# Kernel optimization log

Measured on AMD Instinct MI355X. Metric: run time of the kernel, lower is better.

## Reference

```python
import jax, jax.numpy as jnp
import numpy as np

NH = 16  # num_attention_heads
DH = 64  # attention_head_size
HID = NH * DH
TYPE_VOCAB = 2


def setup_inputs() -> dict:
    key = jax.random.key(0)
    ks = jax.random.split(key, 10)
    B, S = 4, 2048
    s = 0.02
    return {
        "hidden_states": jax.random.normal(ks[0], (B, S, HID), jnp.float32),
        "attention_mask": jnp.zeros((B, 1, 1, S), jnp.float32),
        "seg_ids": jax.random.randint(ks[1], (B, S), 0, TYPE_VOCAB),
        "Wq": jax.random.normal(ks[2], (HID, HID), jnp.float32) * s,
        "bq": jnp.zeros((HID,), jnp.float32),
        "Wk": jax.random.normal(ks[3], (HID, HID), jnp.float32) * s,  # key has NO bias (F.linear with weight only)
        "Wv": jax.random.normal(ks[4], (HID, HID), jnp.float32) * s,
        "bv": jnp.zeros((HID,), jnp.float32),
        "seg_table": jax.random.normal(ks[5], (TYPE_VOCAB, HID), jnp.float32) * s,
        "b_q_s": jnp.zeros((1, NH, 1, DH), jnp.float32),
    }


def reference(hidden_states, attention_mask, seg_ids, Wq, bq, Wk, Wv, bv, seg_table, b_q_s):
    B, S, H = hidden_states.shape
    # QKV projections (key projection has no bias, matching F.linear(x, key.weight))
    q = hidden_states @ Wq.T + bq
    k = hidden_states @ Wk.T
    v = hidden_states @ Wv.T + bv
    # [B, NH, S, DH]
    q = q.reshape(B, S, NH, DH).transpose(0, 2, 1, 3)
    k = k.reshape(B, S, NH, DH).transpose(0, 2, 1, 3)
    v = v.reshape(B, S, NH, DH).transpose(0, 2, 1, 3)
    scale = 1.0 / np.sqrt(DH).astype(np.float32)
    scores = jnp.einsum('bhid,bhjd->bhij', q * scale, k)
    # segment-embedding bias: seg_rep [B, S, NH, DH]
    seg_rep = seg_table[seg_ids].reshape(B, S, NH, DH)
    qs = jnp.einsum('bhid,bjhd->bhij', q + b_q_s, seg_rep)
    scores = scores + qs + attention_mask
    probs = jax.nn.softmax(scores, axis=-1)  # dropout: eval mode (identity)
    ctx = jnp.einsum('bhij,bhjd->bihd', probs, v).reshape(B, S, H)
    return ctx
```

## Files before the change

### kernel.cpp

```cpp
#include <hip/hip_runtime.h>
#include <cstdint>
#include <cmath>

#define RLN2 1.44269504088896340736f

typedef __attribute__((ext_vector_type(8))) short short8;
typedef __attribute__((ext_vector_type(4))) float f32x4;
typedef __attribute__((ext_vector_type(4))) unsigned int uint4v;

__device__ __forceinline__ unsigned short f2bf(float f) {
  unsigned int u = __float_as_uint(f);
  u += 0x7fffu + ((u >> 16) & 1u);
  return (unsigned short)(u >> 16);
}

__device__ __forceinline__ unsigned int cvt_pk_bf16(float lo, float hi) {
  unsigned int r;
  asm("v_cvt_pk_bf16_f32 %0, %1, %2" : "=v"(r) : "v"(lo), "v"(hi));
  return r;
}

__device__ __forceinline__ float fast_exp2(float x) {
#if __has_builtin(__builtin_amdgcn_exp2f)
  return __builtin_amdgcn_exp2f(x);
#else
  return exp2f(x);
#endif
}

__device__ __forceinline__ void gload16(const void* g, void* l) {
  __builtin_amdgcn_global_load_lds(
      (const __attribute__((address_space(1))) unsigned int*)g,
      (__attribute__((address_space(3))) unsigned int*)l,
      16, 0, 0);
}


__global__ void __launch_bounds__(256) k_cvt_hs(const float* __restrict__ src,
                                                unsigned short* __restrict__ dst) {
  size_t i = (size_t)blockIdx.x * 256 + threadIdx.x;
  const float4* s = (const float4*)src + i * 2;
  float4 a = s[0], b = s[1];
  short8 o;
  o[0] = (short)f2bf(a.x); o[1] = (short)f2bf(a.y); o[2] = (short)f2bf(a.z); o[3] = (short)f2bf(a.w);
  o[4] = (short)f2bf(b.x); o[5] = (short)f2bf(b.y); o[6] = (short)f2bf(b.z); o[7] = (short)f2bf(b.w);
  ((short8*)dst)[i] = o;
}

__global__ void __launch_bounds__(256) k_cvt_w(const float* __restrict__ Wq,
                                               const float* __restrict__ Wk,
                                               const float* __restrict__ Wv,
                                               unsigned short* __restrict__ dst) {
  size_t i = (size_t)blockIdx.x * 256 + threadIdx.x;
  int e = (int)(i * 8);
  int n = e >> 10, c = e & 1023;
  const float* row = (n < 1024) ? (Wq + (size_t)n * 1024)
                   : (n < 2048) ? (Wk + (size_t)(n - 1024) * 1024)
                                : (Wv + (size_t)(n - 2048) * 1024);
  const float4* s = (const float4*)(row + c);
  float4 a = s[0], b = s[1];
  short8 o;
  o[0] = (short)f2bf(a.x); o[1] = (short)f2bf(a.y); o[2] = (short)f2bf(a.z); o[3] = (short)f2bf(a.w);
  o[4] = (short)f2bf(b.x); o[5] = (short)f2bf(b.y); o[6] = (short)f2bf(b.z); o[7] = (short)f2bf(b.w);
  ((short8*)dst)[i] = o;
}

__global__ void __launch_bounds__(256) k_seg(const int* __restrict__ seg_ids,
                                             const float* __restrict__ seg_table,
                                             unsigned short* __restrict__ Kaug) {
  size_t i = (size_t)blockIdx.x * 256 + threadIdx.x;
  int e = (int)(i * 8);
  int jl = e >> 10;
  int r  = e & 1023;
  int sid = seg_ids[jl];
  const float4* s = (const float4*)(seg_table + (size_t)sid * 1024 + r);
  float4 a = s[0], b = s[1];
  short8 o;
  o[0] = (short)f2bf(a.x); o[1] = (short)f2bf(a.y); o[2] = (short)f2bf(a.z); o[3] = (short)f2bf(a.w);
  o[4] = (short)f2bf(b.x); o[5] = (short)f2bf(b.y); o[6] = (short)f2bf(b.z); o[7] = (short)f2bf(b.w);
  int b_ = jl >> 11, j = jl & 2047;
  int h = r >> 6, d = r & 63;
  size_t off = ((size_t)(b_ * 16 + h) * 2048 + j) * 128 + 64 + d;
  *(short8*)(Kaug + off) = o;
}

__global__ void __launch_bounds__(256) k_vt(const unsigned short* __restrict__ V,
                                            unsigned short* __restrict__ Vt) {
  __shared__ unsigned short lt[64 * 72];
  int blk = blockIdx.x;
  int bh = blk >> 5, jt = blk & 31;
  int j0 = jt * 64;
  int tid = threadIdx.x;
  const char* src = (const char*)(V + ((size_t)bh * 2048 + j0) * 64);
#pragma unroll
  for (int it = 0; it < 2; ++it) {
    int c = tid + it * 256;
    int j = c >> 3, colb = (c & 7) * 16;
    int jpos = (j & 32) | ((((j >> 2) & 3) << 3) + (((j >> 4) & 1) << 2) + (j & 3));
    short8 v = *(const short8*)(src + (size_t)j * 128 + colb);
    int d0 = colb >> 1;
#pragma unroll
    for (int e = 0; e < 8; ++e)
      lt[(d0 + e) * 72 + jpos] = (unsigned short)v[e];
  }
  __syncthreads();
  char* dst = (char*)(Vt + (size_t)bh * 131072 + j0);
#pragma unroll
  for (int it = 0; it < 2; ++it) {
    int c = tid + it * 256;
    int d = c >> 3, jc = (c & 7) * 8;
    short8 o = *(const short8*)&lt[d * 72 + jc];
    *(short8*)(dst + (size_t)d * 4096 + jc * 2) = o;
  }
}

__global__ void __launch_bounds__(256) k_gemm(const unsigned short* __restrict__ A,
                                              const unsigned short* __restrict__ Bw,
                                              const float* __restrict__ bq,
                                              const float* __restrict__ bv,
                                              const float* __restrict__ bqs,
                                              unsigned short* __restrict__ Qaug,
                                              unsigned short* __restrict__ Kaug,
                                              unsigned short* __restrict__ Vo) {
  __shared__ unsigned short As[128 * 32];
  __shared__ unsigned short Bs[128 * 32];
  int n0 = blockIdx.x * 128;
  int m0 = blockIdx.y * 128;
  int tid = threadIdx.x;
  int w = tid >> 6, lane = tid & 63;
  int wr = (w >> 1) * 64, wc = (w & 1) * 64;
  int rA = lane & 15;
  int kg = (lane >> 4) * 16;
  f32x4 acc[4][4] = {};
  const char* Ab = (const char*)A;
  const char* Bb = (const char*)Bw;

  for (int kt = 0; kt < 32; ++kt) {
    int kb0 = kt * 64;
#pragma unroll
    for (int c = 0; c < 2; ++c) {
      int chunk = w * 2 + c;
      int y = chunk * 1024 + lane * 16;
      int row = y >> 6, colb = y & 63;
      gload16(Ab + (size_t)(m0 + row) * 2048 + kb0 + colb, (char*)As + chunk * 1024);
      gload16(Bb + (size_t)(n0 + row) * 2048 + kb0 + colb, (char*)Bs + chunk * 1024);
    }
    __syncthreads();
    short8 af[4], bfr[4];
#pragma unroll
    for (int m = 0; m < 4; ++m)
      af[m] = *(const short8*)((const char*)As + (wr + m * 16 + rA) * 64 + kg);
#pragma unroll
    for (int n = 0; n < 4; ++n)
      bfr[n] = *(const short8*)((const char*)Bs + (wc + n * 16 + rA) * 64 + kg);
#pragma unroll
    for (int m = 0; m < 4; ++m)
#pragma unroll
      for (int n = 0; n < 4; ++n)
        acc[m][n] = __builtin_amdgcn_mfma_f32_16x16x32_bf16(af[m], bfr[n], acc[m][n], 0, 0, 0);
    __syncthreads();
  }

  int seg = n0 >> 10;
  int colbase = n0 & 1023;
#pragma unroll
  for (int n = 0; n < 4; ++n) {
    int o = colbase + wc + n * 16 + (lane & 15);
    int h = o >> 6, d = o & 63;
    float bias = 0.f, bqsv = 0.f;
    if (seg == 0) { bias = bq[o]; bqsv = bqs[o]; }
    else if (seg == 2) { bias = bv[o]; }
#pragma unroll
    for (int m = 0; m < 4; ++m) {
#pragma unroll
      for (int r = 0; r < 4; ++r) {
        int i = m0 + wr + m * 16 + (lane >> 4) * 4 + r;
        int b_ = i >> 11, sdx = i & 2047;
        float val = acc[m][n][r];
        size_t tok = (size_t)(b_ * 16 + h) * 2048 + sdx;
        if (seg == 0) {
          float qv = val + bias;
          Qaug[tok * 128 + d]      = f2bf(qv * (0.125f * RLN2));
          Qaug[tok * 128 + 64 + d] = f2bf((qv + bqsv) * RLN2);
        } else if (seg == 1) {
          Kaug[tok * 128 + d] = f2bf(val);
        } else {
          Vo[tok * 64 + d] = f2bf(val + bias);
        }
      }
    }
  }
}

__global__ void __launch_bounds__(256, 3) k_attn(const unsigned short* __restrict__ Qaug,
                                                 const unsigned short* __restrict__ Kaug,
                                                 const unsigned short* __restrict__ Vt,
                                                 const float* __restrict__ mask,
                                                 float* __restrict__ out) {
  __shared__ char smem[49152];
  char* Ksb = smem;
  char* Vsb = smem + 32768;

  int qt = blockIdx.x, h = blockIdx.y, b_ = blockIdx.z;
  int bh = b_ * 16 + h;
  int i0 = qt * 64;
  int tid = threadIdx.x, w = tid >> 6, lane = tid & 63;
  int q16 = lane & 15, g = lane >> 4;
  int swzq = (q16 & 7) << 4;
  const char* Qg = (const char*)Qaug + (size_t)bh * 2048 * 256;
  const char* Kg = (const char*)Kaug + (size_t)bh * 2048 * 256;
  const char* Vg = (const char*)Vt + (size_t)bh * 64 * 4096;
  const float* maskb = mask + (size_t)b_ * 2048;

  int kl_row = lane >> 2, kl_cb = (lane & 3) * 16;
  int vl_dvl = lane >> 3, vl_bv = (lane & 7) * 16;

#pragma unroll
  for (int c = 0; c < 4; ++c) {
    int ck = w * 4 + c;
    int db = ck >> 2, rhi = (ck & 3) << 4;
    gload16(Kg + (size_t)(rhi + kl_row) * 256 + db * 64 + kl_cb, Ksb + ck * 1024);
  }
#pragma unroll
  for (int c = 0; c < 2; ++c) {
    int ck = w * 2 + c;
    int dv = ck * 8 + vl_dvl;
    gload16(Vg + (size_t)dv * 4096 + ((vl_bv ^ ((dv & 7) << 4)) & 127), Vsb + ck * 1024);
  }

  short8 qf[4];
  {
    const char* qrow = Qg + (size_t)(i0 + w * 16 + q16) * 256 + g * 16;
#pragma unroll
    for (int db = 0; db < 4; ++db)
      qf[db] = *(const short8*)(qrow + db * 64);
  }
  __syncthreads();

  float m_run = -1e30f, l_run = 0.f;
  f32x4 accO[4] = {};

  for (int t = 0; t < 32; ++t) {
    int cur = t & 1, nxt = cur ^ 1;
    int j0 = t * 64;
    if (t < 31) {
      int jn = j0 + 64;
      char* kd = Ksb + nxt * 16384;
      char* vd = Vsb + nxt * 8192;
#pragma unroll
      for (int c = 0; c < 4; ++c) {
        int ck = w * 4 + c;
        int db = ck >> 2, rhi = (ck & 3) << 4;
        gload16(Kg + (size_t)(jn + rhi + kl_row) * 256 + db * 64 + kl_cb, kd + ck * 1024);
      }
#pragma unroll
      for (int c = 0; c < 2; ++c) {
        int ck = w * 2 + c;
        int dv = ck * 8 + vl_dvl;
        gload16(Vg + (size_t)dv * 4096 + jn * 2 + ((vl_bv ^ ((dv & 7) << 4)) & 127),
                vd + ck * 1024);
      }
    }
    const char* kbase = Ksb + cur * 16384 + q16 * 64 + g * 16;
    const char* vb_ = Vsb + cur * 8192;
    const char* vbase0 = vb_ + ((q16 * 128 + g * 16) ^ swzq);
    const char* vbase1 = vb_ + ((q16 * 128 + 64 + g * 16) ^ swzq);

    f32x4 s[4] = {};
    __builtin_amdgcn_s_setprio(1);
#pragma unroll
    for (int jb = 0; jb < 4; ++jb) {
#pragma unroll
      for (int db = 0; db < 4; ++db) {
        short8 kf = *(const short8*)(kbase + db * 4096 + jb * 1024);
        s[jb] = __builtin_amdgcn_mfma_f32_16x16x32_bf16(kf, qf[db], s[jb], 0, 0, 0);
      }
    }
    __builtin_amdgcn_s_setprio(0);

#pragma unroll
    for (int jb = 0; jb < 4; ++jb) {
      f32x4 mv = *(const f32x4*)(maskb + j0 + jb * 16 + g * 4);
      s[jb] = s[jb] + mv * RLN2;
    }

    float tm = fmaxf(fmaxf(s[0][0], s[0][1]), s[0][2]);
    tm = fmaxf(fmaxf(tm, s[0][3]), fmaxf(s[1][0], s[1][1]));
    tm = fmaxf(fmaxf(tm, s[1][2]), fmaxf(s[1][3], s[2][0]));
    tm = fmaxf(fmaxf(tm, s[2][1]), fmaxf(s[2][2], s[2][3]));
    tm = fmaxf(fmaxf(tm, s[3][0]), fmaxf(s[3][1], s[3][2]));
    tm = fmaxf(tm, s[3][3]);
    tm = fmaxf(tm, __shfl_xor(tm, 16));
    tm = fmaxf(tm, __shfl_xor(tm, 32));

    if (__any(tm > m_run + 8.0f)) {
      float mn = fmaxf(m_run, tm);
      float alpha = fast_exp2(m_run - mn);
      m_run = mn;
      l_run *= alpha;
      float al[4];
#pragma unroll
      for (int r = 0; r < 4; ++r)
        al[r] = __shfl(alpha, (lane & 48) + g * 4 + r);
#pragma unroll
      for (int nb = 0; nb < 4; ++nb) {
        accO[nb][0] *= al[0]; accO[nb][1] *= al[1];
        accO[nb][2] *= al[2]; accO[nb][3] *= al[3];
      }
    }

    f32x4 pssum = {0.f, 0.f, 0.f, 0.f};
#pragma unroll
    for (int jb = 0; jb < 4; ++jb) {
      f32x4 x = s[jb] - m_run;
      f32x4 e;
      e[0] = fast_exp2(x[0]); e[1] = fast_exp2(x[1]);
      e[2] = fast_exp2(x[2]); e[3] = fast_exp2(x[3]);
      s[jb] = e;
      pssum = pssum + e;
    }
    float ps = (pssum[0] + pssum[1]) + (pssum[2] + pssum[3]);
    ps += __shfl_xor(ps, 16);
    ps += __shfl_xor(ps, 32);
    l_run += ps;

    unsigned int pk[4][2];
#pragma unroll
    for (int jb = 0; jb < 4; ++jb) {
      pk[jb][0] = cvt_pk_bf16(s[jb][0], s[jb][1]);
      pk[jb][1] = cvt_pk_bf16(s[jb][2], s[jb][3]);
    }

    __builtin_amdgcn_s_setprio(1);
#pragma unroll
    for (int kb = 0; kb < 2; ++kb) {
      uint4v pw;
      pw[0] = pk[2 * kb][0]; pw[1] = pk[2 * kb][1];
      pw[2] = pk[2 * kb + 1][0]; pw[3] = pk[2 * kb + 1][1];
      short8 pf = __builtin_bit_cast(short8, pw);
      const char* vbase = kb ? vbase1 : vbase0;
#pragma unroll
      for (int nb = 0; nb < 4; ++nb) {
        short8 vf = *(const short8*)(vbase + nb * 2048);
        accO[nb] = __builtin_amdgcn_mfma_f32_16x16x32_bf16(pf, vf, accO[nb], 0, 0, 0);
      }
    }
    __builtin_amdgcn_s_setprio(0);
    __syncthreads();
  }

  float lr[4];
#pragma unroll
  for (int r = 0; r < 4; ++r)
    lr[r] = 1.0f / __shfl(l_run, (lane & 48) + g * 4 + r);
#pragma unroll
  for (int nb = 0; nb < 4; ++nb) {
    int dv = nb * 16 + q16;
#pragma unroll
    for (int r = 0; r < 4; ++r) {
      int i = i0 + w * 16 + g * 4 + r;
      out[((size_t)b_ * 2048 + i) * 1024 + h * 64 + dv] = accO[nb][r] * lr[r];
    }
  }
}

extern "C" void kernel_launch(void* const* d_in, const int* in_sizes, int n_in,
                              void* d_out, int out_size, void* d_ws, size_t ws_size,
                              hipStream_t stream) {
  (void)in_sizes; (void)n_in; (void)out_size; (void)ws_size;
  const float* hs        = (const float*)d_in[0];
  const float* mask      = (const float*)d_in[1];
  const int*   seg_ids   = (const int*)d_in[2];
  const float* Wq        = (const float*)d_in[3];
  const float* bq        = (const float*)d_in[4];
  const float* Wk        = (const float*)d_in[5];
  const float* Wv        = (const float*)d_in[6];
  const float* bv        = (const float*)d_in[7];
  const float* seg_table = (const float*)d_in[8];
  const float* bqs       = (const float*)d_in[9];
  float* out = (float*)d_out;
  char* ws = (char*)d_ws;

  unsigned short* hsb  = (unsigned short*)(ws + 0);
  unsigned short* Wcat = (unsigned short*)(ws + 16777216);
  unsigned short* Qaug = (unsigned short*)(ws + 23068672);
  unsigned short* Kaug = (unsigned short*)(ws + 56623104);
  unsigned short* V    = (unsigned short*)(ws + 90177536);
  unsigned short* Vt   = (unsigned short*)(ws + 0);

  k_cvt_hs<<<dim3(4096), dim3(256), 0, stream>>>(hs, hsb);
  k_cvt_w<<<dim3(1536), dim3(256), 0, stream>>>(Wq, Wk, Wv, Wcat);
  k_gemm<<<dim3(24, 64), dim3(256), 0, stream>>>(hsb, Wcat, bq, bv, bqs, Qaug, Kaug, V);
  k_seg<<<dim3(4096), dim3(256), 0, stream>>>(seg_ids, seg_table, Kaug);
  k_vt<<<dim3(2048), dim3(256), 0, stream>>>(V, Vt);
  k_attn<<<dim3(32, 16, 4), dim3(256), 0, stream>>>(Qaug, Kaug, Vt, mask, out);
}
```

Baseline: 297.7 us.

## Switch attention kernel to 32x32x16 MFMA with 128-row query tiles

Rewrites the attention inner loop to use 32x32x16 bf16 MFMA instead of 16x16x32, with each wave handling 32 query rows, so the block covers 128 queries and the grid is halved. The K/V shared-memory layouts, swizzles and V transpose ordering are changed to match the new fragment shapes, and output stores become vectorised float4 writes. Row statistics now need only one cross-lane shuffle, and per-row alpha/l broadcasts disappear. This halves K/V reloads per query and cuts softmax shuffle work, at the cost of more registers per thread (two 16-float accumulators plus scores) and fewer blocks, which may lower occupancy.

```diff
diff --git a/kernel.cpp b/kernel.cpp
--- a/kernel.cpp
+++ b/kernel.cpp
@@ -6,6 +6,7 @@
 
 typedef __attribute__((ext_vector_type(8))) short short8;
 typedef __attribute__((ext_vector_type(4))) float f32x4;
+typedef __attribute__((ext_vector_type(16))) float f32x16;
 typedef __attribute__((ext_vector_type(4))) unsigned int uint4v;
 
 __device__ __forceinline__ unsigned short f2bf(float f) {
@@ -96,7 +97,8 @@
   for (int it = 0; it < 2; ++it) {
     int c = tid + it * 256;
     int j = c >> 3, colb = (c & 7) * 16;
-    int jpos = (j & 32) | ((((j >> 2) & 3) << 3) + (((j >> 4) & 1) << 2) + (j & 3));
+    int kh2 = (j >> 5) & 1, c2 = (j >> 3) & 3, hi2 = (j >> 2) & 1, r2 = j & 3;
+    int jpos = (2 * kh2 + (c2 >> 1)) * 16 + 8 * hi2 + 4 * (c2 & 1) + r2;
     short8 v = *(const short8*)(src + (size_t)j * 128 + colb);
     int d0 = colb >> 1;
 #pragma unroll
@@ -203,42 +205,48 @@
 
   int qt = blockIdx.x, h = blockIdx.y, b_ = blockIdx.z;
   int bh = b_ * 16 + h;
-  int i0 = qt * 64;
+  int i0 = qt * 128;
   int tid = threadIdx.x, w = tid >> 6, lane = tid & 63;
-  int q16 = lane & 15, g = lane >> 4;
-  int swzq = (q16 & 7) << 4;
+  int q = lane & 31, hi = lane >> 5;
+  int swzq = (q & 7) << 4;
   const char* Qg = (const char*)Qaug + (size_t)bh * 2048 * 256;
   const char* Kg = (const char*)Kaug + (size_t)bh * 2048 * 256;
   const char* Vg = (const char*)Vt + (size_t)bh * 64 * 4096;
   const float* maskb = mask + (size_t)b_ * 2048;
 
-  int kl_row = lane >> 2, kl_cb = (lane & 3) * 16;
-  int vl_dvl = lane >> 3, vl_bv = (lane & 7) * 16;
+  int foff[8];
+#pragma unroll
+  for (int ds = 0; ds < 8; ++ds)
+    foff[ds] = (ds * 32 + hi * 16) ^ swzq;
+
+  int kst_row = lane >> 4, kst_x = (lane & 15) * 16;
+  int vst_dv = lane >> 3;
+  int vst_x = ((lane & 7) * 16) ^ ((vst_dv & 7) << 4);
 
 #pragma unroll
   for (int c = 0; c < 4; ++c) {
     int ck = w * 4 + c;
-    int db = ck >> 2, rhi = (ck & 3) << 4;
-    gload16(Kg + (size_t)(rhi + kl_row) * 256 + db * 64 + kl_cb, Ksb + ck * 1024);
+    int krow = ck * 4 + kst_row;
+    gload16(Kg + (size_t)krow * 256 + (kst_x ^ ((krow & 7) << 4)), Ksb + ck * 1024);
   }
 #pragma unroll
   for (int c = 0; c < 2; ++c) {
     int ck = w * 2 + c;
-    int dv = ck * 8 + vl_dvl;
-    gload16(Vg + (size_t)dv * 4096 + ((vl_bv ^ ((dv & 7) << 4)) & 127), Vsb + ck * 1024);
-  }
-
-  short8 qf[4];
+    int dv = ck * 8 + vst_dv;
+    gload16(Vg + (size_t)dv * 4096 + vst_x, Vsb + ck * 1024);
+  }
+
+  short8 qf[8];
   {
-    const char* qrow = Qg + (size_t)(i0 + w * 16 + q16) * 256 + g * 16;
-#pragma unroll
-    for (int db = 0; db < 4; ++db)
-      qf[db] = *(const short8*)(qrow + db * 64);
+    const char* qrow = Qg + (size_t)(i0 + w * 32 + q) * 256 + hi * 16;
+#pragma unroll
+    for (int ds = 0; ds < 8; ++ds)
+      qf[ds] = *(const short8*)(qrow + ds * 32);
   }
   __syncthreads();
 
   float m_run = -1e30f, l_run = 0.f;
-  f32x4 accO[4] = {};
+  f32x16 accO[2] = {};
 
   for (int t = 0; t < 32; ++t) {
     int cur = t & 1, nxt = cur ^ 1;
@@ -250,47 +258,44 @@
 #pragma unroll
       for (int c = 0; c < 4; ++c) {
         int ck = w * 4 + c;
-        int db = ck >> 2, rhi = (ck & 3) << 4;
-        gload16(Kg + (size_t)(jn + rhi + kl_row) * 256 + db * 64 + kl_cb, kd + ck * 1024);
+        int krow = ck * 4 + kst_row;
+        gload16(Kg + (size_t)(jn + krow) * 256 + (kst_x ^ ((krow & 7) << 4)), kd + ck * 1024);
       }
 #pragma unroll
       for (int c = 0; c < 2; ++c) {
         int ck = w * 2 + c;
-        int dv = ck * 8 + vl_dvl;
-        gload16(Vg + (size_t)dv * 4096 + jn * 2 + ((vl_bv ^ ((dv & 7) << 4)) & 127),
-                vd + ck * 1024);
+        int dv = ck * 8 + vst_dv;
+        gload16(Vg + (size_t)dv * 4096 + jn * 2 + vst_x, vd + ck * 1024);
       }
     }
-    const char* kbase = Ksb + cur * 16384 + q16 * 64 + g * 16;
-    const char* vb_ = Vsb + cur * 8192;
-    const char* vbase0 = vb_ + ((q16 * 128 + g * 16) ^ swzq);
-    const char* vbase1 = vb_ + ((q16 * 128 + 64 + g * 16) ^ swzq);
-
-    f32x4 s[4] = {};
+    const char* kq = Ksb + cur * 16384 + q * 256;
+    const char* vq = Vsb + cur * 8192 + q * 128;
+
+    f32x16 s0 = {}, s1 = {};
     __builtin_amdgcn_s_setprio(1);
 #pragma unroll
-    for (int jb = 0; jb < 4; ++jb) {
-#pragma unroll
-      for (int db = 0; db < 4; ++db) {
-        short8 kf = *(const short8*)(kbase + db * 4096 + jb * 1024);
-        s[jb] = __builtin_amdgcn_mfma_f32_16x16x32_bf16(kf, qf[db], s[jb], 0, 0, 0);
+    for (int ds = 0; ds < 8; ++ds) {
+      short8 kf0 = *(const short8*)(kq + foff[ds]);
+      short8 kf1 = *(const short8*)(kq + foff[ds] + 8192);
+      s0 = __builtin_amdgcn_mfma_f32_32x32x16_bf16(kf0, qf[ds], s0, 0, 0, 0);
+      s1 = __builtin_amdgcn_mfma_f32_32x32x16_bf16(kf1, qf[ds], s1, 0, 0, 0);
+    }
+    __builtin_amdgcn_s_setprio(0);
+
+#pragma unroll
+    for (int c = 0; c < 4; ++c) {
+      f32x4 mv0 = *(const f32x4*)(maskb + j0 + 8 * c + 4 * hi);
+      f32x4 mv1 = *(const f32x4*)(maskb + j0 + 32 + 8 * c + 4 * hi);
+#pragma unroll
+      for (int r = 0; r < 4; ++r) {
+        s0[4 * c + r] += mv0[r] * RLN2;
+        s1[4 * c + r] += mv1[r] * RLN2;
       }
     }
-    __builtin_amdgcn_s_setprio(0);
-
-#pragma unroll
-    for (int jb = 0; jb < 4; ++jb) {
-      f32x4 mv = *(const f32x4*)(maskb + j0 + jb * 16 + g * 4);
-      s[jb] = s[jb] + mv * RLN2;
-    }
-
-    float tm = fmaxf(fmaxf(s[0][0], s[0][1]), s[0][2]);
-    tm = fmaxf(fmaxf(tm, s[0][3]), fmaxf(s[1][0], s[1][1]));
-    tm = fmaxf(fmaxf(tm, s[1][2]), fmaxf(s[1][3], s[2][0]));
-    tm = fmaxf(fmaxf(tm, s[2][1]), fmaxf(s[2][2], s[2][3]));
-    tm = fmaxf(fmaxf(tm, s[3][0]), fmaxf(s[3][1], s[3][2]));
-    tm = fmaxf(tm, s[3][3]);
-    tm = fmaxf(tm, __shfl_xor(tm, 16));
+
+    float tm = -1e30f;
+#pragma unroll
+    for (int i = 0; i < 16; ++i) tm = fmaxf(tm, fmaxf(s0[i], s1[i]));
     tm = fmaxf(tm, __shfl_xor(tm, 32));
 
     if (__any(tm > m_run + 8.0f)) {
@@ -298,68 +303,57 @@
       float alpha = fast_exp2(m_run - mn);
       m_run = mn;
       l_run *= alpha;
-      float al[4];
-#pragma unroll
-      for (int r = 0; r < 4; ++r)
-        al[r] = __shfl(alpha, (lane & 48) + g * 4 + r);
-#pragma unroll
-      for (int nb = 0; nb < 4; ++nb) {
-        accO[nb][0] *= al[0]; accO[nb][1] *= al[1];
-        accO[nb][2] *= al[2]; accO[nb][3] *= al[3];
-      }
-    }
-
-    f32x4 pssum = {0.f, 0.f, 0.f, 0.f};
-#pragma unroll
-    for (int jb = 0; jb < 4; ++jb) {
-      f32x4 x = s[jb] - m_run;
-      f32x4 e;
-      e[0] = fast_exp2(x[0]); e[1] = fast_exp2(x[1]);
-      e[2] = fast_exp2(x[2]); e[3] = fast_exp2(x[3]);
-      s[jb] = e;
-      pssum = pssum + e;
-    }
-    float ps = (pssum[0] + pssum[1]) + (pssum[2] + pssum[3]);
-    ps += __shfl_xor(ps, 16);
+#pragma unroll
+      for (int i = 0; i < 16; ++i) { accO[0][i] *= alpha; accO[1][i] *= alpha; }
+    }
+
+    float ps = 0.f;
+#pragma unroll
+    for (int i = 0; i < 16; ++i) {
+      float e0 = fast_exp2(s0[i] - m_run);
+      float e1 = fast_exp2(s1[i] - m_run);
+      s0[i] = e0; s1[i] = e1;
+      ps += e0 + e1;
+    }
     ps += __shfl_xor(ps, 32);
     l_run += ps;
 
-    unsigned int pk[4][2];
-#pragma unroll
-    for (int jb = 0; jb < 4; ++jb) {
-      pk[jb][0] = cvt_pk_bf16(s[jb][0], s[jb][1]);
-      pk[jb][1] = cvt_pk_bf16(s[jb][2], s[jb][3]);
+    uint4v pk[4];
+#pragma unroll
+    for (int ks = 0; ks < 4; ++ks) {
+      int o = 8 * (ks & 1);
+      const f32x16& sv = (ks < 2) ? s0 : s1;
+      pk[ks][0] = cvt_pk_bf16(sv[o + 0], sv[o + 1]);
+      pk[ks][1] = cvt_pk_bf16(sv[o + 2], sv[o + 3]);
+      pk[ks][2] = cvt_pk_bf16(sv[o + 4], sv[o + 5]);
+      pk[ks][3] = cvt_pk_bf16(sv[o + 6], sv[o + 7]);
     }
 
     __builtin_amdgcn_s_setprio(1);
 #pragma unroll
-    for (int kb = 0; kb < 2; ++kb) {
-      uint4v pw;
-      pw[0] = pk[2 * kb][0]; pw[1] = pk[2 * kb][1];
-      pw[2] = pk[2 * kb + 1][0]; pw[3] = pk[2 * kb + 1][1];
-      short8 pf = __builtin_bit_cast(short8, pw);
-      const char* vbase = kb ? vbase1 : vbase0;
-#pragma unroll
-      for (int nb = 0; nb < 4; ++nb) {
-        short8 vf = *(const short8*)(vbase + nb * 2048);
-        accO[nb] = __builtin_amdgcn_mfma_f32_16x16x32_bf16(pf, vf, accO[nb], 0, 0, 0);
-      }
+    for (int ks = 0; ks < 4; ++ks) {
+      short8 pf = __builtin_bit_cast(short8, pk[ks]);
+      short8 vf0 = *(const short8*)(vq + foff[ks]);
+      short8 vf1 = *(const short8*)(vq + foff[ks] + 4096);
+      accO[0] = __builtin_amdgcn_mfma_f32_32x32x16_bf16(vf0, pf, accO[0], 0, 0, 0);
+      accO[1] = __builtin_amdgcn_mfma_f32_32x32x16_bf16(vf1, pf, accO[1], 0, 0, 0);
     }
     __builtin_amdgcn_s_setprio(0);
     __syncthreads();
   }
 
-  float lr[4];
-#pragma unroll
-  for (int r = 0; r < 4; ++r)
-    lr[r] = 1.0f / __shfl(l_run, (lane & 48) + g * 4 + r);
-#pragma unroll
-  for (int nb = 0; nb < 4; ++nb) {
-    int dv = nb * 16 + q16;
-#pragma unroll
-    for (int r = 0; r < 4; ++r) {
-      int i = i0 + w * 16 + g * 4 + r;
-      out[((size_t)b_ * 2048 + i) * 1024 + h * 64 + dv] = accO[nb][r] * lr[r];
+  float inv = 1.0f / l_run;
+  float* orow = out + ((size_t)b_ * 2048 + i0 + w * 32 + q) * 1024 + h * 64;
+#pragma unroll
+  for (int vh = 0; vh < 2; ++vh) {
+#pragma unroll
+    for (int c = 0; c < 4; ++c) {
+      f32x4 o;
+      o[0] = accO[vh][4 * c + 0] * inv;
+      o[1] = accO[vh][4 * c + 1] * inv;
+      o[2] = accO[vh][4 * c + 2] * inv;
+      o[3] = accO[vh][4 * c + 3] * inv;
+      *(f32x4*)(orow + vh * 32 + 8 * c + 4 * hi) = o;
     }
   }
 }
@@ -393,5 +387,5 @@
   k_gemm<<<dim3(24, 64), dim3(256), 0, stream>>>(hsb, Wcat, bq, bv, bqs, Qaug, Kaug, V);
   k_seg<<<dim3(4096), dim3(256), 0, stream>>>(seg_ids, seg_table, Kaug);
   k_vt<<<dim3(2048), dim3(256), 0, stream>>>(V, Vt);
-  k_attn<<<dim3(32, 16, 4), dim3(256), 0, stream>>>(Qaug, Kaug, Vt, mask, out);
-}
+  k_attn<<<dim3(16, 16, 4), dim3(256), 0, stream>>>(Qaug, Kaug, Vt, mask, out);
+}
```

Result: faster. 280.4 us (-5.8%).
